# Performance work log

Measured on AMD Instinct MI355X. Metric: run time of the kernel, lower is better.

Reference implementation:

```python
import jax, jax.numpy as jnp
import numpy as np

NUM_GRAPHS = 1024

def setup_inputs() -> dict:
    key = jax.random.key(0)
    ks = jax.random.split(key, 6)
    N, E = 500000, 16000000
    x = jax.random.normal(ks[0], (N, 4), dtype=jnp.float32)
    edge_index = jax.random.randint(ks[1], (2, E), 0, N, dtype=jnp.int32)
    batch = jnp.sort(jax.random.randint(ks[2], (N,), 0, NUM_GRAPHS, dtype=jnp.int32))
    eps = jnp.zeros((), dtype=jnp.float32)
    W1 = jax.random.normal(ks[3], (4, 16), dtype=jnp.float32) * 0.5
    b1 = jnp.zeros((16,), dtype=jnp.float32)
    W2 = jax.random.normal(ks[4], (16, 4), dtype=jnp.float32) * 0.25
    b2 = jnp.zeros((4,), dtype=jnp.float32)
    return {"x": x, "edge_index": edge_index, "batch": batch,
            "eps": eps, "W1": W1, "b1": b1, "W2": W2, "b2": b2}

def reference(x, edge_index, batch, eps, W1, b1, W2, b2):
    N = x.shape[0]
    src, dst = edge_index[0], edge_index[1]
    # GINConv aggregation: sum of neighbor (source) features at each target node
    agg = jax.ops.segment_sum(x[src], dst, num_segments=N)  # [N, 4]
    h = (1.0 + eps) * x + agg
    # 2-layer MLP: Lin(4,16) -> ReLU -> Lin(16,4)
    h = jax.nn.relu(h @ W1 + b1) @ W2 + b2
    h = jax.nn.relu(h)
    # global_mean_pool over batch segment ids
    sums = jax.ops.segment_sum(h, batch, num_segments=NUM_GRAPHS)      # [G, 4]
    cnts = jax.ops.segment_sum(jnp.ones((N,), h.dtype), batch, num_segments=NUM_GRAPHS)
    pooled = sums / jnp.maximum(cnts, 1.0)[:, None]
    return jax.nn.log_softmax(pooled, axis=1)
```

## Files before the change

### kernel.cpp

```cpp
#include <hip/hip_runtime.h>

#define NUM_GRAPHS 1024
#define BIN_BITS 10
#define BIN_SIZE (1 << BIN_BITS)
#define EB 4096
#define STH 512
#define EPT 8
#define SWAVES 8
#define CURS 16
#define ACCTH 256
#define ACCW 4

typedef int v4i __attribute__((ext_vector_type(4)));

__device__ inline unsigned bf16_rn(float f) {
    unsigned u = __float_as_uint(f);
    return (u + 0x7FFFu + ((u >> 16) & 1u)) >> 16;
}
__global__ void prep_kernel(const float4* __restrict__ x, uint2* __restrict__ x16,
                            int N, int* __restrict__ cursor,
                            float* __restrict__ gsum, float* __restrict__ gcnt,
                            int cap) {
    int i = blockIdx.x * blockDim.x + threadIdx.x;
    if (i < 512) cursor[i * CURS] = i * cap;
    if (i < NUM_GRAPHS * 4) gsum[i] = 0.0f;
    if (i < NUM_GRAPHS) gcnt[i] = 0.0f;
    if (i < N) {
        float4 v = x[i];
        uint2 r;
        r.x = bf16_rn(v.x) | (bf16_rn(v.y) << 16);
        r.y = bf16_rn(v.z) | (bf16_rn(v.w) << 16);
        x16[i] = r;
    }
}

__global__ void __launch_bounds__(STH, 6) bin_scatter(const int* __restrict__ src,
                                                      const int* __restrict__ dst,
                                                      int* __restrict__ packed,
                                                      int* __restrict__ cursor,
                                                      int E, int cap, int nb) {
    __shared__ int hist[SWAVES][512];
    __shared__ int wbase[SWAVES][512];

    const int t = threadIdx.x;
    const int lane = t & 63;
    const int wave = t >> 6;
    const int b0 = blockIdx.x * EB;
    const int myBase = b0 + t * EPT;

    for (int j = t; j < SWAVES * 512; j += STH) (&hist[0][0])[j] = 0;
    __syncthreads();

    int dbuf[EPT], sbuf[EPT];
    const bool full = (myBase + EPT <= E);
    if (full) {
        *(int4*)(dbuf)     = *(const int4*)(dst + myBase);
        *(int4*)(dbuf + 4) = *(const int4*)(dst + myBase + 4);
        *(int4*)(sbuf)     = *(const int4*)(src + myBase);
        *(int4*)(sbuf + 4) = *(const int4*)(src + myBase + 4);
    } else {
#pragma unroll
        for (int i = 0; i < EPT; ++i) {
            int e = myBase + i;
            bool ok = e < E;
            dbuf[i] = ok ? dst[e] : 0;
            sbuf[i] = ok ? src[e] : 0;
        }
    }

    int pv[EPT];
    int bnlp[EPT];
#pragma unroll
    for (int k = 0; k < EPT; ++k) {
        int e = myBase + k;
        bool ok = full || (e < E);
        int d = dbuf[k];
        int bn = ((unsigned)d) >> BIN_BITS;
        pv[k] = ((d & (BIN_SIZE - 1)) << 19) | sbuf[k];
        unsigned long long m = __ballot(ok);
#pragma unroll
        for (int bb = 0; bb < 9; ++bb) {
            unsigned long long bm = __ballot((bn >> bb) & 1);
            m &= ((bn >> bb) & 1) ? bm : ~bm;
        }
        int rank = (int)__popcll(m & ((1ull << lane) - 1ull));
        int cnt  = (int)__popcll(m);
        int leader = __ffsll((unsigned long long)m) - 1;
        int old = hist[wave][bn];
        if (ok && lane == leader) hist[wave][bn] = old + cnt;
        bnlp[k] = ok ? ((bn << 16) | (old + rank)) : -1;
    }
    __syncthreads();

    {
        int c[SWAVES];
        int total = 0;
#pragma unroll
        for (int w = 0; w < SWAVES; ++w) { c[w] = hist[w][t]; total += c[w]; }
        int base = 0;
        if (t < nb && total > 0) base = atomicAdd(&cursor[t * CURS], total);
        int acc = base;
#pragma unroll
        for (int w = 0; w < SWAVES; ++w) { wbase[w][t] = acc; acc += c[w]; }
    }
    __syncthreads();

    if (full) {
#pragma unroll
        for (int k = 0; k < EPT; ++k) {
            int bn = ((unsigned)bnlp[k]) >> 16;
            int lp = bnlp[k] & 0xFFFF;
            int pos = wbase[wave][bn] + lp;
            if (pos < (bn + 1) * cap)
                packed[pos] = pv[k];
        }
    } else {
#pragma unroll
        for (int k = 0; k < EPT; ++k) {
            if (bnlp[k] >= 0) {
                int bn = ((unsigned)bnlp[k]) >> 16;
                int lp = bnlp[k] & 0xFFFF;
                int pos = wbase[wave][bn] + lp;
                if (pos < (bn + 1) * cap)
                    packed[pos] = pv[k];
            }
        }
    }
}

__global__ void __launch_bounds__(ACCTH) bin_accum_mlp_pool(
        const float4* __restrict__ x,
        const uint2* __restrict__ x16,
        const int* __restrict__ packed,
        const int* __restrict__ cursor,
        const int* __restrict__ batch,
        const float* __restrict__ eps_p,
        const float* __restrict__ W1, const float* __restrict__ b1,
        const float* __restrict__ W2, const float* __restrict__ b2,
        float* __restrict__ gsum, float* __restrict__ gcnt,
        int N, int cap) {
    __shared__ float planes[ACCW][BIN_SIZE][4];

    const int bin = blockIdx.x;
    const int t = threadIdx.x;
    const int lane = t & 63;
    const int wave = t >> 6;

    {
        float4* pz = (float4*)&planes[0][0][0];
        float4 z; z.x = 0.f; z.y = 0.f; z.z = 0.f; z.w = 0.f;
#pragma unroll
        for (int i = 0; i < 16; ++i) pz[t + i * ACCTH] = z;
    }
    __syncthreads();

    const int start = bin * cap;
    int end = cursor[bin * CURS];
    if (end > start + cap) end = start + cap;
    int cnt = end - start; if (cnt < 0) cnt = 0;

    int seg = ((cnt + ACCW - 1) / ACCW + 3) & ~3;
    int s0 = start + wave * seg;
    int s1 = s0 + seg; if (s1 > end) s1 = end;

    for (int base = s0; base < s1; base += 256) {
        int b = base + lane * 4;
        int pe[4];
        if (b + 3 < s1) {
            v4i p4 = __builtin_nontemporal_load((const v4i*)(packed + b));
            pe[0] = p4.x; pe[1] = p4.y; pe[2] = p4.z; pe[3] = p4.w;
        } else {
            pe[0] = (b + 0 < s1) ? packed[b + 0] : -1;
            pe[1] = (b + 1 < s1) ? packed[b + 1] : -1;
            pe[2] = (b + 2 < s1) ? packed[b + 2] : -1;
            pe[3] = (b + 3 < s1) ? packed[b + 3] : -1;
        }
        uint2 g[4];
#pragma unroll
        for (int k = 0; k < 4; ++k) g[k] = x16[pe[k] & 0x7FFFF];

#pragma unroll
        for (int k = 0; k < 4; ++k) {
            int p = pe[k];
            bool ok = p >= 0;
            int dl = (((unsigned)p) >> 19) & (BIN_SIZE - 1);
            unsigned long long m;
            {
                unsigned long long bv = __ballot(ok);
                m = ok ? bv : ~bv;
#pragma unroll
                for (int bb = 0; bb < BIN_BITS; ++bb) {
                    unsigned long long bl_ = __ballot((dl >> bb) & 1);
                    m &= ((dl >> bb) & 1) ? bl_ : ~bl_;
                }
            }
            int rank = ok ? (int)__popcll(m & ((1ull << lane) - 1ull)) : -1;

            float v0 = __uint_as_float(g[k].x << 16);
            float v1 = __uint_as_float(g[k].x & 0xFFFF0000u);
            float v2 = __uint_as_float(g[k].y << 16);
            float v3 = __uint_as_float(g[k].y & 0xFFFF0000u);
            float4* pp = (float4*)&planes[wave][dl][0];
            for (int pass = 0; __any(rank >= pass); ++pass) {
                if (rank == pass) {
                    float4 a = *pp;
                    a.x += v0; a.y += v1; a.z += v2; a.w += v3;
                    *pp = a;
                }
            }
        }
    }
    __syncthreads();

    const float eps = eps_p[0];
    for (int half = 0; half < 4; ++half) {
        int node = t + half * ACCTH;
        float4 a = *(const float4*)&planes[0][node][0];
#pragma unroll
        for (int w = 1; w < ACCW; ++w) {
            float4 bq = *(const float4*)&planes[w][node][0];
            a.x += bq.x; a.y += bq.y; a.z += bq.z; a.w += bq.w;
        }

        int n = bin * BIN_SIZE + node;
        bool valid = n < N;
        float o0 = 0.f, o1 = 0.f, o2 = 0.f, o3 = 0.f;
        int g = -1;
        if (valid) {
            float4 xv = x[n];
            float h0 = (1.0f + eps) * xv.x + a.x;
            float h1 = (1.0f + eps) * xv.y + a.y;
            float h2 = (1.0f + eps) * xv.z + a.z;
            float h3 = (1.0f + eps) * xv.w + a.w;

            float tmp[16];
#pragma unroll
            for (int j = 0; j < 16; ++j) {
                float v = b1[j] + h0 * W1[j] + h1 * W1[16 + j] + h2 * W1[32 + j] + h3 * W1[48 + j];
                tmp[j] = v > 0.0f ? v : 0.0f;
            }
            float o[4];
#pragma unroll
            for (int j = 0; j < 4; ++j) {
                float v = b2[j];
#pragma unroll
                for (int k = 0; k < 16; ++k) v += tmp[k] * W2[k * 4 + j];
                o[j] = v > 0.0f ? v : 0.0f;
            }
            o0 = o[0]; o1 = o[1]; o2 = o[2]; o3 = o[3];
            g = batch[n];
        }

        int g0 = __shfl(g, 0);
        bool uni = __all(g == g0);
        if (uni && g0 >= 0) {
#pragma unroll
            for (int off = 32; off > 0; off >>= 1) {
                o0 += __shfl_down(o0, off);
                o1 += __shfl_down(o1, off);
                o2 += __shfl_down(o2, off);
                o3 += __shfl_down(o3, off);
            }
            if (lane == 0) {
                unsafeAtomicAdd(&gsum[(size_t)g0 * 4 + 0], o0);
                unsafeAtomicAdd(&gsum[(size_t)g0 * 4 + 1], o1);
                unsafeAtomicAdd(&gsum[(size_t)g0 * 4 + 2], o2);
                unsafeAtomicAdd(&gsum[(size_t)g0 * 4 + 3], o3);
                unsafeAtomicAdd(&gcnt[g0], 64.0f);
            }
        } else if (valid) {
            unsafeAtomicAdd(&gsum[(size_t)g * 4 + 0], o0);
            unsafeAtomicAdd(&gsum[(size_t)g * 4 + 1], o1);
            unsafeAtomicAdd(&gsum[(size_t)g * 4 + 2], o2);
            unsafeAtomicAdd(&gsum[(size_t)g * 4 + 3], o3);
            unsafeAtomicAdd(&gcnt[g], 1.0f);
        }
    }
}

__global__ void pool_softmax_kernel(const float* __restrict__ gsum,
                                    const float* __restrict__ gcnt,
                                    float* __restrict__ out) {
    int g = blockIdx.x * blockDim.x + threadIdx.x;
    if (g >= NUM_GRAPHS) return;
    float c = fmaxf(gcnt[g], 1.0f);
    float p0 = gsum[g * 4 + 0] / c;
    float p1 = gsum[g * 4 + 1] / c;
    float p2 = gsum[g * 4 + 2] / c;
    float p3 = gsum[g * 4 + 3] / c;
    float m = fmaxf(fmaxf(p0, p1), fmaxf(p2, p3));
    float s = expf(p0 - m) + expf(p1 - m) + expf(p2 - m) + expf(p3 - m);
    float lse = m + logf(s);
    out[g * 4 + 0] = p0 - lse;
    out[g * 4 + 1] = p1 - lse;
    out[g * 4 + 2] = p2 - lse;
    out[g * 4 + 3] = p3 - lse;
}

__global__ void edge_scatter_kernel(const float4* __restrict__ x,
                                    const int* __restrict__ src,
                                    const int* __restrict__ dst,
                                    float* __restrict__ agg,
                                    int E) {
    int t = blockIdx.x * blockDim.x + threadIdx.x;
    int e = t * 4;
    if (e + 3 < E) {
        int4 s = *(const int4*)(src + e);
        int4 d = *(const int4*)(dst + e);
        float4 xv;
        xv = x[s.x];
        unsafeAtomicAdd(&agg[(size_t)d.x * 4 + 0], xv.x);
        unsafeAtomicAdd(&agg[(size_t)d.x * 4 + 1], xv.y);
        unsafeAtomicAdd(&agg[(size_t)d.x * 4 + 2], xv.z);
        unsafeAtomicAdd(&agg[(size_t)d.x * 4 + 3], xv.w);
        xv = x[s.y];
        unsafeAtomicAdd(&agg[(size_t)d.y * 4 + 0], xv.x);
        unsafeAtomicAdd(&agg[(size_t)d.y * 4 + 1], xv.y);
        unsafeAtomicAdd(&agg[(size_t)d.y * 4 + 2], xv.z);
        unsafeAtomicAdd(&agg[(size_t)d.y * 4 + 3], xv.w);
        xv = x[s.z];
        unsafeAtomicAdd(&agg[(size_t)d.z * 4 + 0], xv.x);
        unsafeAtomicAdd(&agg[(size_t)d.z * 4 + 1], xv.y);
        unsafeAtomicAdd(&agg[(size_t)d.z * 4 + 2], xv.z);
        unsafeAtomicAdd(&agg[(size_t)d.z * 4 + 3], xv.w);
        xv = x[s.w];
        unsafeAtomicAdd(&agg[(size_t)d.w * 4 + 0], xv.x);
        unsafeAtomicAdd(&agg[(size_t)d.w * 4 + 1], xv.y);
        unsafeAtomicAdd(&agg[(size_t)d.w * 4 + 2], xv.z);
        unsafeAtomicAdd(&agg[(size_t)d.w * 4 + 3], xv.w);
    } else {
        for (int i = e; i < E; ++i) {
            int sv = src[i], dv = dst[i];
            float4 xv = x[sv];
            unsafeAtomicAdd(&agg[(size_t)dv * 4 + 0], xv.x);
            unsafeAtomicAdd(&agg[(size_t)dv * 4 + 1], xv.y);
            unsafeAtomicAdd(&agg[(size_t)dv * 4 + 2], xv.z);
            unsafeAtomicAdd(&agg[(size_t)dv * 4 + 3], xv.w);
        }
    }
}

__global__ void node_mlp_pool_kernel(const float4* __restrict__ x,
                                     const float4* __restrict__ agg,
                                     const int* __restrict__ batch,
                                     const float* __restrict__ eps_p,
                                     const float* __restrict__ W1,
                                     const float* __restrict__ b1,
                                     const float* __restrict__ W2,
                                     const float* __restrict__ b2,
                                     float* __restrict__ gsum,
                                     float* __restrict__ gcnt,
                                     int N) {
    int i = blockIdx.x * blockDim.x + threadIdx.x;
    bool valid = i < N;
    float o0 = 0.f, o1 = 0.f, o2 = 0.f, o3 = 0.f;
    int g = -1;
    if (valid) {
        float eps = eps_p[0];
        float4 xv = x[i];
        float4 av = agg[i];
        float h0 = (1.0f + eps) * xv.x + av.x;
        float h1 = (1.0f + eps) * xv.y + av.y;
        float h2 = (1.0f + eps) * xv.z + av.z;
        float h3 = (1.0f + eps) * xv.w + av.w;
        float tmp[16];
#pragma unroll
        for (int j = 0; j < 16; ++j) {
            float v = b1[j] + h0 * W1[j] + h1 * W1[16 + j] + h2 * W1[32 + j] + h3 * W1[48 + j];
            tmp[j] = v > 0.0f ? v : 0.0f;
        }
        float o[4];
#pragma unroll
        for (int j = 0; j < 4; ++j) {
            float v = b2[j];
#pragma unroll
            for (int k = 0; k < 16; ++k) v += tmp[k] * W2[k * 4 + j];
            o[j] = v > 0.0f ? v : 0.0f;
        }
        o0 = o[0]; o1 = o[1]; o2 = o[2]; o3 = o[3];
        g = batch[i];
    }
    int g0 = __shfl(g, 0);
    bool uni = __all(g == g0);
    if (uni && g0 >= 0) {
#pragma unroll
        for (int off = 32; off > 0; off >>= 1) {
            o0 += __shfl_down(o0, off);
            o1 += __shfl_down(o1, off);
            o2 += __shfl_down(o2, off);
            o3 += __shfl_down(o3, off);
        }
        if ((threadIdx.x & 63) == 0) {
            unsafeAtomicAdd(&gsum[(size_t)g0 * 4 + 0], o0);
            unsafeAtomicAdd(&gsum[(size_t)g0 * 4 + 1], o1);
            unsafeAtomicAdd(&gsum[(size_t)g0 * 4 + 2], o2);
            unsafeAtomicAdd(&gsum[(size_t)g0 * 4 + 3], o3);
            unsafeAtomicAdd(&gcnt[g0], 64.0f);
        }
    } else if (valid) {
        unsafeAtomicAdd(&gsum[(size_t)g * 4 + 0], o0);
        unsafeAtomicAdd(&gsum[(size_t)g * 4 + 1], o1);
        unsafeAtomicAdd(&gsum[(size_t)g * 4 + 2], o2);
        unsafeAtomicAdd(&gsum[(size_t)g * 4 + 3], o3);
        unsafeAtomicAdd(&gcnt[g], 1.0f);
    }
}

extern "C" void kernel_launch(void* const* d_in, const int* in_sizes, int n_in,
                              void* d_out, int out_size, void* d_ws, size_t ws_size,
                              hipStream_t stream) {
    const float* x     = (const float*)d_in[0];
    const int*   ei    = (const int*)d_in[1];
    const int*   batch = (const int*)d_in[2];
    const float* eps   = (const float*)d_in[3];
    const float* W1    = (const float*)d_in[4];
    const float* b1    = (const float*)d_in[5];
    const float* W2    = (const float*)d_in[6];
    const float* b2    = (const float*)d_in[7];

    const int N = in_sizes[0] / 4;
    const int E = in_sizes[1] / 2;
    const int* src = ei;
    const int* dst = ei + (size_t)E;

    const int nb = (N + BIN_SIZE - 1) >> BIN_BITS;
    const int epb = (E + nb - 1) / nb;
    int cap = epb + epb / 8 + 1024;
    cap = (cap + 3) & ~3;

    size_t x16_elems = ((size_t)2 * N + 3) & ~(size_t)3;
    size_t packed_elems = ((size_t)nb * cap + 3) & ~(size_t)3;
    size_t need = (x16_elems + packed_elems + 512 * CURS + NUM_GRAPHS * 5) * sizeof(float);

    if (nb <= 512 && N < (1 << 19) && need <= ws_size) {
        uint2* x16    = (uint2*)d_ws;
        int*   packed = (int*)d_ws + x16_elems;
        int*   cursor = packed + packed_elems;
        float* gsum   = (float*)(cursor + 512 * CURS);
        float* gcnt   = gsum + (size_t)NUM_GRAPHS * 4;

        prep_kernel<<<(N + 511) / 512, 512, 0, stream>>>(
            (const float4*)x, x16, N, cursor, gsum, gcnt, cap);

        int nblocks_e = (E + EB - 1) / EB;
        bin_scatter<<<nblocks_e, STH, 0, stream>>>(src, dst, packed, cursor, E, cap, nb);

        bin_accum_mlp_pool<<<nb, ACCTH, 0, stream>>>(
            (const float4*)x, (const uint2*)x16, packed, cursor, batch, eps,
            W1, b1, W2, b2, gsum, gcnt, N, cap);

        pool_softmax_kernel<<<(NUM_GRAPHS + 255) / 256, 256, 0, stream>>>(
            gsum, gcnt, (float*)d_out);
    } else {
        float* agg  = (float*)d_ws;
        float* gsum = agg + (size_t)N * 4;
        float* gcnt = gsum + (size_t)NUM_GRAPHS * 4;
        size_t zero_bytes = ((size_t)N * 4 + NUM_GRAPHS * 5) * sizeof(float);
        (void)hipMemsetAsync(d_ws, 0, zero_bytes, stream);

        int e4 = (E + 3) / 4;
        edge_scatter_kernel<<<(e4 + 255) / 256, 256, 0, stream>>>(
            (const float4*)x, src, dst, agg, E);

        node_mlp_pool_kernel<<<(N + 255) / 256, 256, 0, stream>>>(
            (const float4*)x, (const float4*)agg, batch, eps, W1, b1, W2, b2,
            gsum, gcnt, N);

        pool_softmax_kernel<<<(NUM_GRAPHS + 255) / 256, 256, 0, stream>>>(
            gsum, gcnt, (float*)d_out);
    }
}
```

Measured before the change: 429.7 us.

## Drop bf16 prep kernel, gather fp32 x directly with double-buffered loads

Removes the prep kernel that converted x to bf16 and initialized cursors, replacing it with a memset and making the cursors relative counts offset by bin*cap. The accumulation loop now gathers fp32 x directly and software-pipelines the next chunk's packed-index load and gather while processing the current one. Invalid lanes are masked by multiplying by zero instead of a separate ballot. This saves a full pass over x and a kernel launch, but doubles the gather bytes per edge and raises register pressure from the double buffering.

```diff
diff --git a/kernel.cpp b/kernel.cpp
--- a/kernel.cpp
+++ b/kernel.cpp
@@ -13,27 +13,6 @@
 
 typedef int v4i __attribute__((ext_vector_type(4)));
 
-__device__ inline unsigned bf16_rn(float f) {
-    unsigned u = __float_as_uint(f);
-    return (u + 0x7FFFu + ((u >> 16) & 1u)) >> 16;
-}
-__global__ void prep_kernel(const float4* __restrict__ x, uint2* __restrict__ x16,
-                            int N, int* __restrict__ cursor,
-                            float* __restrict__ gsum, float* __restrict__ gcnt,
-                            int cap) {
-    int i = blockIdx.x * blockDim.x + threadIdx.x;
-    if (i < 512) cursor[i * CURS] = i * cap;
-    if (i < NUM_GRAPHS * 4) gsum[i] = 0.0f;
-    if (i < NUM_GRAPHS) gcnt[i] = 0.0f;
-    if (i < N) {
-        float4 v = x[i];
-        uint2 r;
-        r.x = bf16_rn(v.x) | (bf16_rn(v.y) << 16);
-        r.y = bf16_rn(v.z) | (bf16_rn(v.w) << 16);
-        x16[i] = r;
-    }
-}
-
 __global__ void __launch_bounds__(STH, 6) bin_scatter(const int* __restrict__ src,
                                                       const int* __restrict__ dst,
                                                       int* __restrict__ packed,
@@ -97,8 +76,8 @@
         int total = 0;
 #pragma unroll
         for (int w = 0; w < SWAVES; ++w) { c[w] = hist[w][t]; total += c[w]; }
-        int base = 0;
-        if (t < nb && total > 0) base = atomicAdd(&cursor[t * CURS], total);
+        int base = t * cap;
+        if (t < nb && total > 0) base += atomicAdd(&cursor[t * CURS], total);
         int acc = base;
 #pragma unroll
         for (int w = 0; w < SWAVES; ++w) { wbase[w][t] = acc; acc += c[w]; }
@@ -128,9 +107,56 @@
     }
 }
 
+#define LOADR(B, PE, VM) do {                                              \
+    int _i = (B) + lane * 4;                                               \
+    if (_i + 3 < s1) {                                                     \
+        v4i _p4 = __builtin_nontemporal_load((const v4i*)(packed + _i));   \
+        PE[0] = _p4.x; PE[1] = _p4.y; PE[2] = _p4.z; PE[3] = _p4.w;        \
+        VM = 0xF;                                                          \
+    } else {                                                               \
+        VM = 0;                                                            \
+        PE[0] = (_i + 0 < s1) ? (VM |= 1, packed[_i + 0]) : 0;             \
+        PE[1] = (_i + 1 < s1) ? (VM |= 2, packed[_i + 1]) : 0;             \
+        PE[2] = (_i + 2 < s1) ? (VM |= 4, packed[_i + 2]) : 0;             \
+        PE[3] = (_i + 3 < s1) ? (VM |= 8, packed[_i + 3]) : 0;             \
+    }                                                                      \
+} while (0)
+
+#define GATHR(PE, G) do {                                                  \
+    G[0] = x[min(PE[0] & 0x7FFFF, N - 1)];                                 \
+    G[1] = x[min(PE[1] & 0x7FFFF, N - 1)];                                 \
+    G[2] = x[min(PE[2] & 0x7FFFF, N - 1)];                                 \
+    G[3] = x[min(PE[3] & 0x7FFFF, N - 1)];                                 \
+} while (0)
+
+#define PROCR(PE, G, VM) do {                                              \
+    _Pragma("unroll")                                                      \
+    for (int k = 0; k < 4; ++k) {                                          \
+        int p = PE[k];                                                     \
+        int dl = (((unsigned)p) >> 19) & (BIN_SIZE - 1);                   \
+        unsigned long long m = ~0ull;                                      \
+        _Pragma("unroll")                                                  \
+        for (int bb = 0; bb < BIN_BITS; ++bb) {                            \
+            unsigned long long bm = __ballot((dl >> bb) & 1);              \
+            m &= ((dl >> bb) & 1) ? bm : ~bm;                              \
+        }                                                                  \
+        int rank = (int)__popcll(m & ((1ull << lane) - 1ull));             \
+        float sc = ((VM >> k) & 1) ? 1.0f : 0.0f;                          \
+        float v0 = G[k].x * sc, v1 = G[k].y * sc;                          \
+        float v2 = G[k].z * sc, v3 = G[k].w * sc;                          \
+        float4* pp = (float4*)&planes[wave][dl][0];                        \
+        for (int pass = 0; __any(rank >= pass); ++pass) {                  \
+            if (rank == pass) {                                            \
+                float4 a = *pp;                                            \
+                a.x += v0; a.y += v1; a.z += v2; a.w += v3;                \
+                *pp = a;                                                   \
+            }                                                              \
+        }                                                                  \
+    }                                                                      \
+} while (0)
+
 __global__ void __launch_bounds__(ACCTH) bin_accum_mlp_pool(
         const float4* __restrict__ x,
-        const uint2* __restrict__ x16,
         const int* __restrict__ packed,
         const int* __restrict__ cursor,
         const int* __restrict__ batch,
@@ -155,59 +181,31 @@
     __syncthreads();
 
     const int start = bin * cap;
-    int end = cursor[bin * CURS];
-    if (end > start + cap) end = start + cap;
-    int cnt = end - start; if (cnt < 0) cnt = 0;
+    int cnt = cursor[bin * CURS];
+    if (cnt > cap) cnt = cap;
+    if (cnt < 0) cnt = 0;
+    const int end = start + cnt;
 
     int seg = ((cnt + ACCW - 1) / ACCW + 3) & ~3;
     int s0 = start + wave * seg;
     int s1 = s0 + seg; if (s1 > end) s1 = end;
 
-    for (int base = s0; base < s1; base += 256) {
-        int b = base + lane * 4;
-        int pe[4];
-        if (b + 3 < s1) {
-            v4i p4 = __builtin_nontemporal_load((const v4i*)(packed + b));
-            pe[0] = p4.x; pe[1] = p4.y; pe[2] = p4.z; pe[3] = p4.w;
-        } else {
-            pe[0] = (b + 0 < s1) ? packed[b + 0] : -1;
-            pe[1] = (b + 1 < s1) ? packed[b + 1] : -1;
-            pe[2] = (b + 2 < s1) ? packed[b + 2] : -1;
-            pe[3] = (b + 3 < s1) ? packed[b + 3] : -1;
-        }
-        uint2 g[4];
-#pragma unroll
-        for (int k = 0; k < 4; ++k) g[k] = x16[pe[k] & 0x7FFFF];
-
-#pragma unroll
-        for (int k = 0; k < 4; ++k) {
-            int p = pe[k];
-            bool ok = p >= 0;
-            int dl = (((unsigned)p) >> 19) & (BIN_SIZE - 1);
-            unsigned long long m;
-            {
-                unsigned long long bv = __ballot(ok);
-                m = ok ? bv : ~bv;
-#pragma unroll
-                for (int bb = 0; bb < BIN_BITS; ++bb) {
-                    unsigned long long bl_ = __ballot((dl >> bb) & 1);
-                    m &= ((dl >> bb) & 1) ? bl_ : ~bl_;
-                }
-            }
-            int rank = ok ? (int)__popcll(m & ((1ull << lane) - 1ull)) : -1;
-
-            float v0 = __uint_as_float(g[k].x << 16);
-            float v1 = __uint_as_float(g[k].x & 0xFFFF0000u);
-            float v2 = __uint_as_float(g[k].y << 16);
-            float v3 = __uint_as_float(g[k].y & 0xFFFF0000u);
-            float4* pp = (float4*)&planes[wave][dl][0];
-            for (int pass = 0; __any(rank >= pass); ++pass) {
-                if (rank == pass) {
-                    float4 a = *pp;
-                    a.x += v0; a.y += v1; a.z += v2; a.w += v3;
-                    *pp = a;
-                }
-            }
+    if (s0 < s1) {
+        int peA[4], peB[4], vmA, vmB;
+        float4 gA[4], gB[4];
+        int b = s0;
+        LOADR(b, peA, vmA);
+        GATHR(peA, gA);
+        for (;;) {
+            int b1n = b + 256;
+            if (b1n < s1) { LOADR(b1n, peB, vmB); GATHR(peB, gB); }
+            PROCR(peA, gA, vmA);
+            if (b1n >= s1) break;
+            int b2n = b1n + 256;
+            if (b2n < s1) { LOADR(b2n, peA, vmA); GATHR(peA, gA); }
+            PROCR(peB, gB, vmB);
+            if (b2n >= s1) break;
+            b = b2n;
         }
     }
     __syncthreads();
@@ -428,25 +426,23 @@
     int cap = epb + epb / 8 + 1024;
     cap = (cap + 3) & ~3;
 
-    size_t x16_elems = ((size_t)2 * N + 3) & ~(size_t)3;
     size_t packed_elems = ((size_t)nb * cap + 3) & ~(size_t)3;
-    size_t need = (x16_elems + packed_elems + 512 * CURS + NUM_GRAPHS * 5) * sizeof(float);
+    size_t need = (packed_elems + 512 * CURS + NUM_GRAPHS * 5) * sizeof(float);
 
     if (nb <= 512 && N < (1 << 19) && need <= ws_size) {
-        uint2* x16    = (uint2*)d_ws;
-        int*   packed = (int*)d_ws + x16_elems;
+        int*   packed = (int*)d_ws;
         int*   cursor = packed + packed_elems;
         float* gsum   = (float*)(cursor + 512 * CURS);
         float* gcnt   = gsum + (size_t)NUM_GRAPHS * 4;
 
-        prep_kernel<<<(N + 511) / 512, 512, 0, stream>>>(
-            (const float4*)x, x16, N, cursor, gsum, gcnt, cap);
+        (void)hipMemsetAsync(cursor, 0,
+                             (512 * CURS + NUM_GRAPHS * 5) * sizeof(int), stream);
 
         int nblocks_e = (E + EB - 1) / EB;
         bin_scatter<<<nblocks_e, STH, 0, stream>>>(src, dst, packed, cursor, E, cap, nb);
 
         bin_accum_mlp_pool<<<nb, ACCTH, 0, stream>>>(
-            (const float4*)x, (const uint2*)x16, packed, cursor, batch, eps,
+            (const float4*)x, packed, cursor, batch, eps,
             W1, b1, W2, b2, gsum, gcnt, N, cap);
 
         pool_softmax_kernel<<<(NUM_GRAPHS + 255) / 256, 256, 0, stream>>>(
```

Result: slower. 495.6 us (+15.3%).
